# Performance work log

Measured on AMD Instinct MI355X. Metric: run time of the kernel, lower is better.

Reference implementation:

```python
import jax, jax.numpy as jnp
import numpy as np

N0, N1, N2 = 1500, 6000, 4000
F_IN, F_OUT = 32, 32
K00, K0P = 2, 2
K1N, K11, K12, K1P = 2, 2, 2, 2
K2N, K22 = 2, 2


def chebyshev(L, k, x):
    # Chebyshev recursion: T1 = L x, T2 = 2 L T1 - x, T_j = 2 L T_{j-1} - T_{j-2}
    # Returns (n, F, k) stack of T1..Tk (identity term handled by caller).
    t_prev = L @ x
    terms = [t_prev]
    t_pp = x
    for _ in range(k - 1):
        t = 2.0 * (L @ t_prev) - t_pp
        t_pp, t_prev = t_prev, t
        terms.append(t)
    return jnp.stack(terms, axis=2)


def _sym(key, n):
    a = jax.random.normal(key, (n, n), jnp.float32) / jnp.sqrt(jnp.float32(n))
    return 0.5 * (a + a.T)


def setup_inputs():
    key = jax.random.key(0)
    ks = jax.random.split(key, 16)
    x0 = jax.random.normal(ks[0], (N0, F_IN), jnp.float32)
    x1 = jax.random.normal(ks[1], (N1, F_IN), jnp.float32)
    x2 = jax.random.normal(ks[2], (N2, F_IN), jnp.float32)
    B1 = jax.random.normal(ks[3], (N0, N1), jnp.float32) / jnp.sqrt(jnp.float32(N1))
    B2 = jax.random.normal(ks[4], (N1, N2), jnp.float32) / jnp.sqrt(jnp.float32(N2))
    L0 = _sym(ks[5], N0)
    L1l = _sym(ks[6], N1)
    L1u = _sym(ks[7], N1)
    L2 = _sym(ks[8], N2)
    # Degree matrices: diagonal with strictly positive entries (as in real SC data).
    D1 = jnp.diag(jax.random.uniform(ks[9], (N0,), jnp.float32, 0.5, 2.0))
    D2 = jnp.diag(jax.random.uniform(ks[10], (N1,), jnp.float32, 0.5, 2.0))
    D3 = jnp.diag(jax.random.uniform(ks[11], (N2,), jnp.float32, 0.5, 2.0))
    D5 = jnp.diag(jax.random.uniform(ks[12], (N1,), jnp.float32, 0.5, 2.0))
    W0 = jax.random.normal(ks[13], (F_IN, F_OUT, 1 + K00 + 1 + K0P), jnp.float32) * 0.05
    W1 = jax.random.normal(ks[14], (F_IN, F_OUT, 1 + K1N + 1 + K11 + K12 + 1 + K1P), jnp.float32) * 0.05
    W2 = jax.random.normal(ks[15], (F_IN, F_OUT, 1 + K2N + 1 + K22), jnp.float32) * 0.05
    return dict(x0=x0, x1=x1, x2=x2, B1=B1, B2=B2, L0=L0, L1l=L1l, L1u=L1u,
                L2=L2, D1=D1, D2=D2, D3=D3, D5=D5, W0=W0, W1=W1, W2=W2)


def _forward(x0, x1, x2, B1, B2, L0, L1l, L1u, L2, d1_inv, d2, d3, d5_pinv, W0, W1, W2):
    # ---- order 0 ----
    x0p = d1_inv[:, None] * (B1 @ x1)               # inv(D1) @ B1 @ x1
    X0 = jnp.concatenate([x0[:, :, None], chebyshev(L0, K00, x0),
                          x0p[:, :, None], chebyshev(L0, K0P, x0p)], axis=2)
    # ---- order 1 ----
    x1n = d2[:, None] * (B1.T @ (d1_inv[:, None] * x0))  # D2 @ B1.T @ inv(D1) @ x0
    x1p = B2 @ (d3[:, None] * x2)                        # B2 @ D3 @ x2
    X1 = jnp.concatenate([x1n[:, :, None], chebyshev(L1l, K1N, x1n),
                          x1[:, :, None], chebyshev(L1l, K11, x1), chebyshev(L1u, K12, x1),
                          x1p[:, :, None], chebyshev(L1u, K1P, x1p)], axis=2)
    # ---- order 2 ----
    x2n = B2.T @ (d5_pinv[:, None] * x1)                 # B2.T @ pinv(D5) @ x1
    X2 = jnp.concatenate([x2n[:, :, None], chebyshev(L2, K2N, x2n),
                          x2[:, :, None], chebyshev(L2, K22, x2)], axis=2)
    y0 = jax.nn.relu(jnp.einsum('nik,iok->no', X0, W0))
    y1 = jax.nn.relu(jnp.einsum('nik,iok->no', X1, W1))
    y2 = jax.nn.relu(jnp.einsum('nik,iok->no', X2, W2))
    return (y0, y1, y2)


def reference(x0, x1, x2, B1, B2, L0, L1l, L1u, L2, D1, D2, D3, D5, W0, W1, W2):
    # D matrices are diagonal degree matrices; inverse/pinverse of a diagonal
    # matrix is the diagonal of (safe) reciprocals -- identical math to
    # torch.inverse / torch.pinverse on these inputs, without an O(n^3) solve.
    d1_inv = 1.0 / jnp.diag(D1)
    d2 = jnp.diag(D2)
    d3 = jnp.diag(D3)
    d5 = jnp.diag(D5)
    d5_pinv = jnp.where(d5 != 0, 1.0 / d5, 0.0)
    return _forward(x0, x1, x2, B1, B2, L0, L1l, L1u, L2, d1_inv, d2, d3, d5_pinv, W0, W1, W2)
```

## Files before the change

kernel.cpp:

```cpp
#include <hip/hip_runtime.h>
#include <stdint.h>

typedef __attribute__((ext_vector_type(4))) float f32x4;
typedef __attribute__((ext_vector_type(8))) short s16x8;
typedef unsigned short us;

static __device__ __forceinline__ us f2bf(float f) {
  union { float f; uint32_t u; } v; v.f = f;
  uint32_t u = v.u;
  u += 0x7fffu + ((u >> 16) & 1u);
  return (us)(u >> 16);
}

static __device__ __forceinline__ float dval(const float* dv, long r, long dstr, int mode) {
  if (!dv || mode == 0) return 1.f;
  float d = dv[r * dstr];
  if (mode == 2) return (d != 0.f) ? 1.f / d : 0.f;
  return d;
}

static __device__ void tpose_tile(const float* __restrict__ src, long lds_, int n,
                                  const float* __restrict__ dv, long dstr, int mode,
                                  us* __restrict__ dst, int ldn, int tile,
                                  us (*sm)[72]) {
  const int t = threadIdx.x;
  const int r0 = tile * 64;
  {
    const int rr = t & 63;
    const int cg = t >> 6;
    const int gr = r0 + rr;
    float sc = 1.f;
    f32x4 v0 = {0.f, 0.f, 0.f, 0.f}, v1 = {0.f, 0.f, 0.f, 0.f};
    if (gr < n) {
      sc = dval(dv, gr, dstr, mode);
      const float* sp = src + (long)gr * lds_ + cg * 8;
      v0 = *(const f32x4*)sp;
      v1 = *(const f32x4*)(sp + 4);
    }
#pragma unroll
    for (int j = 0; j < 4; ++j) {
      sm[cg * 8 + j][rr] = f2bf(v0[j] * sc);
      sm[cg * 8 + 4 + j][rr] = f2bf(v1[j] * sc);
    }
  }
  __syncthreads();
  {
    const int f = t >> 3;
    const int nc = (t & 7) * 8;
    if (r0 + nc < ldn) {
      s16x8 v = *(const s16x8*)&sm[f][nc];
      *(s16x8*)(dst + (size_t)f * ldn + r0 + nc) = v;
    }
  }
}

static __device__ void convT_tile(const float* __restrict__ in, int ldi, int nI, int nC,
                                  us* __restrict__ outT, int ldoT, int bx, int by,
                                  us (*sT)[72]) {
  const int t = threadIdx.x;
  const int tc0 = bx * 64;
  const int tr0 = by * 64;
  const int c0 = (t & 15) * 4;
  const int r0 = (t >> 4) * 4;
  us ub[4][4];
#pragma unroll
  for (int j = 0; j < 4; ++j) {
    int gr = tr0 + r0 + j;
    f32x4 v = {0.f, 0.f, 0.f, 0.f};
    if (gr < nI) {
      const float* pI = in + (size_t)gr * ldi + tc0 + c0;
      if (tc0 + c0 + 3 < nC) {
        v = *(const f32x4*)pI;
      } else {
#pragma unroll
        for (int jj = 0; jj < 4; ++jj) if (tc0 + c0 + jj < nC) v[jj] = pI[jj];
      }
    }
#pragma unroll
    for (int jj = 0; jj < 4; ++jj) ub[j][jj] = f2bf(v[jj]);
  }
#pragma unroll
  for (int jj = 0; jj < 4; ++jj) {
    union { us u[4]; unsigned long long ll; } w;
#pragma unroll
    for (int j = 0; j < 4; ++j) w.u[j] = ub[j][jj];
    *(unsigned long long*)&sT[c0 + jj][r0] = w.ll;
  }
  __syncthreads();
#pragma unroll
  for (int p = 0; p < 2; ++p) {
    int orow = (t >> 3) + p * 32;
    int rcol = (t & 7) * 8;
    int grow = tc0 + orow;
    int gcol = tr0 + rcol;
    if (grow < nC && gcol < ldoT) {
      union { unsigned long long ll[2]; s16x8 v; } w;
      w.ll[0] = *(const unsigned long long*)&sT[orow][rcol];
      w.ll[1] = *(const unsigned long long*)&sT[orow][rcol + 4];
      *(s16x8*)(outT + (size_t)grow * ldoT + gcol) = w.v;
    }
  }
}

struct TSeg { const float* src; us* dst; int lds_, n, ldn, start; };
struct TPack { TSeg t[8]; int nseg; };

__global__ __launch_bounds__(256) void tpose_batch(TPack P) {
  __shared__ us sm[32][72];
  int b = blockIdx.x;
  int si = P.nseg - 1;
  while (si > 0 && P.t[si].start > b) --si;
  const TSeg s = P.t[si];
  tpose_tile(s.src, s.lds_, s.n, nullptr, 0, 0, s.dst, s.ldn, b - s.start, sm);
}

__global__ __launch_bounds__(256) void prep(
    const float* __restrict__ x0, const float* __restrict__ x1, const float* __restrict__ x2,
    const float* __restrict__ D1, const float* __restrict__ D3, const float* __restrict__ D5,
    const float* __restrict__ W0, const float* __restrict__ W1, const float* __restrict__ W2,
    us* x0T, us* x0dT, us* x1T, us* x1dT, us* x2T, us* x2dT,
    us* W0T, us* W1T, us* W2T,
    float* __restrict__ X0a, float* __restrict__ X1a, float* __restrict__ X2a) {
  __shared__ us sm[32][72];
  int b = blockIdx.x;
  if (b < 24)  { tpose_tile(x0, 32, 1500, nullptr, 0, 0, x0T, 1536, b, sm); return; }
  b -= 24;
  if (b < 24)  { tpose_tile(x0, 32, 1500, D1, 1501, 2, x0dT, 1536, b, sm); return; }
  b -= 24;
  if (b < 94)  { tpose_tile(x1, 32, 6000, nullptr, 0, 0, x1T, 6016, b, sm); return; }
  b -= 94;
  if (b < 94)  { tpose_tile(x1, 32, 6000, D5, 6001, 2, x1dT, 6016, b, sm); return; }
  b -= 94;
  if (b < 64)  { tpose_tile(x2, 32, 4000, nullptr, 0, 0, x2T, 4096, b, sm); return; }
  b -= 64;
  if (b < 64)  { tpose_tile(x2, 32, 4000, D3, 4001, 1, x2dT, 4096, b, sm); return; }
  b -= 64;
  if (b < 3) {
    const float* W = (b == 0) ? W0 : ((b == 1) ? W1 : W2);
    us* dst = (b == 0) ? W0T : ((b == 1) ? W1T : W2T);
    const int K = (b == 1) ? 11 : 6;
    const int C = K * 32;
    const int CP = (b == 1) ? 384 : 192;
    for (int idx = threadIdx.x; idx < 32 * CP; idx += 256) {
      int o = idx / CP, j = idx - o * CP;
      float v = 0.f;
      if (j < C) { int k = j >> 5, i = j & 31; v = W[((long)i * 32 + o) * K + k]; }
      dst[(size_t)o * CP + j] = f2bf(v);
    }
    return;
  }
  b -= 3;
  const long V0 = 1500L * 48, V1 = 6000L * 88, V2 = 4000L * 48;
  for (long i = (long)b * 256 + threadIdx.x; i < V0 + V1 + V2; i += 512L * 256) {
    f32x4 v = {0.f, 0.f, 0.f, 0.f};
    float* dst;
    if (i < V0) {
      long r = i / 48; int c0 = (int)(i - r * 48) * 4;
      if (c0 < 32) v = *(const f32x4*)(x0 + r * 32 + c0);
      dst = X0a + r * 192 + c0;
    } else if (i < V0 + V1) {
      long j = i - V0; long r = j / 88; int c0 = (int)(j - r * 88) * 4;
      if (c0 >= 96 && c0 < 128) v = *(const f32x4*)(x1 + r * 32 + (c0 - 96));
      dst = X1a + r * 352 + c0;
    } else {
      long j = i - V0 - V1; long r = j / 48; int c0 = (int)(j - r * 48) * 4;
      if (c0 >= 96 && c0 < 128) v = *(const f32x4*)(x2 + r * 32 + (c0 - 96));
      dst = X2a + r * 192 + c0;
    }
    *(f32x4*)dst = v;
  }
}

struct Seg {
  const void* A; us* Aout;
  const us* Bt0; const us* Bt1;
  const float* S0; const float* S1; const float* sv;
  float* C0; float* C1;
  float alpha, beta;
  int lda, ldao, ldS, sstr, ldc;
  int n_rows, n_k, ldb, smode, kchunk, tiles, ky, start;
};
struct CSeg { const float* in; us* out; int ldi, nI, nC, ldoT, cx, start; };
struct Mega {
  Seg s[4]; CSeg c[2]; TSeg t[2];
  int nseg, gemm_end, nconv, conv_end, ntp;
};

template <int F, int KSTEP, bool RELU, typename AT>
__global__ __launch_bounds__(256) void mega(Mega P) {
  constexpr int NV = KSTEP / 32;
  __shared__ __align__(16) us lds[64 * (KSTEP == 128 ? 256 : 128)];
  const int b = blockIdx.x;
  if (b >= P.gemm_end) {
    if (b < P.conv_end) {
      int lb = b - P.gemm_end;
      int si = P.nconv - 1;
      while (si > 0 && P.c[si].start > lb) --si;
      const CSeg s = P.c[si];
      int l = lb - s.start;
      convT_tile(s.in, s.ldi, s.nI, s.nC, s.out, s.ldoT, l % s.cx, l / s.cx, (us(*)[72])lds);
    } else {
      int lb = b - P.conv_end;
      int si = P.ntp - 1;
      while (si > 0 && P.t[si].start > lb) --si;
      const TSeg s = P.t[si];
      tpose_tile(s.src, s.lds_, s.n, nullptr, 0, 0, s.dst, s.ldn, lb - s.start, (us(*)[72])lds);
    }
    return;
  }

  us* sA = lds;
  us* sX = lds + 64 * KSTEP;

  int si = P.nseg - 1;
  while (si > 0 && P.s[si].start > b) --si;
  const Seg sg = P.s[si];
  const int local = b - sg.start;
  const int bx = local % sg.tiles;
  const int kidx = local / sg.tiles;

  const AT* __restrict__ A = (const AT*)sg.A;
  const int n_rows = sg.n_rows, n_k = sg.n_k, ldb = sg.ldb;

  const int tid = threadIdx.x;
  const int k_begin = kidx * sg.kchunk;
  const int k_end = min(n_k, k_begin + sg.kchunk);
  const int nsteps = (k_end - k_begin + KSTEP - 1) / KSTEP;

  const int srow = tid >> 2;
  const int sslot = tid & 3;
  const int kc_off = sslot * (KSTEP / 4);
  const long arowg = (long)bx * 64 + srow;
  const bool arow_ok = arowg < n_rows;
  const bool xrow_ok = (F == 64) || (srow < 32);
  const us* xbase = ((srow < 32) ? sg.Bt0 : sg.Bt1) + (size_t)(srow & 31) * ldb;

  f32x4 af[KSTEP / 16];
  s16x8 abf[NV];
  s16x8 xr[NV];

  auto load_tiles = [&](int k0) {
    int kc = k0 + kc_off;
    if constexpr (sizeof(AT) == 4) {
#pragma unroll
      for (int h = 0; h < KSTEP / 16; ++h) af[h] = f32x4{0.f, 0.f, 0.f, 0.f};
      if (arow_ok) {
        const float* ap = (const float*)A + (size_t)arowg * sg.lda + kc;
        if (kc + KSTEP / 4 <= n_k) {
#pragma unroll
          for (int h = 0; h < KSTEP / 16; ++h) af[h] = *(const f32x4*)(ap + 4 * h);
        } else {
#pragma unroll
          for (int h = 0; h < KSTEP / 16; ++h)
#pragma unroll
            for (int j = 0; j < 4; ++j)
              if (kc + 4 * h + j < n_k) af[h][j] = ap[4 * h + j];
        }
      }
    } else {
#pragma unroll
      for (int h = 0; h < NV; ++h) abf[h] = (s16x8)0;
      if (arow_ok) {
        const us* ap = (const us*)A + (size_t)arowg * sg.lda + kc;
        if (kc + KSTEP / 4 <= n_k) {
#pragma unroll
          for (int h = 0; h < NV; ++h) abf[h] = *(const s16x8*)(ap + 8 * h);
        } else {
#pragma unroll
          for (int h = 0; h < NV; ++h)
#pragma unroll
            for (int j = 0; j < 8; ++j)
              if (kc + 8 * h + j < n_k) abf[h][j] = (short)ap[8 * h + j];
        }
      }
    }
    if (xrow_ok) {
#pragma unroll
      for (int h = 0; h < NV; ++h) xr[h] = *(const s16x8*)(xbase + kc + 8 * h);
    }
  };

  load_tiles(k_begin);

  const int wave = tid >> 6;
  const int lane = tid & 63;
  const int g = lane >> 4;
  const int r = lane & 15;

  f32x4 acc[F / 16];
#pragma unroll
  for (int i = 0; i < F / 16; ++i) acc[i] = f32x4{0.f, 0.f, 0.f, 0.f};

  for (int s = 0; s < nsteps; ++s) {
#pragma unroll
    for (int h = 0; h < NV; ++h) {
      s16x8 pk;
      if constexpr (sizeof(AT) == 4) {
#pragma unroll
        for (int j = 0; j < 4; ++j) {
          pk[j] = (short)f2bf(af[2 * h][j]);
          pk[4 + j] = (short)f2bf(af[2 * h + 1][j]);
        }
        if (sg.Aout && arow_ok) {
          *(s16x8*)(sg.Aout + (size_t)arowg * sg.ldao + (k_begin + s * KSTEP + kc_off) + 8 * h) = pk;
        }
      } else {
        pk = abf[h];
      }
      const int ws = ((NV * sslot + h) ^ (srow & 7)) * 8;
      *(s16x8*)&sA[srow * KSTEP + ws] = pk;
      if (xrow_ok) *(s16x8*)&sX[srow * KSTEP + ws] = xr[h];
    }
    __syncthreads();
    if (s + 1 < nsteps) load_tiles(k_begin + (s + 1) * KSTEP);

    const int arow = wave * 16 + r;
#pragma unroll
    for (int kk = 0; kk < NV; ++kk) {
      s16x8 afr = *(s16x8*)&sA[arow * KSTEP + (((kk * 4 + g) ^ (arow & 7)) << 3)];
#pragma unroll
      for (int nt = 0; nt < F / 16; ++nt) {
        int xc = nt * 16 + r;
        s16x8 bfr = *(s16x8*)&sX[xc * KSTEP + (((kk * 4 + g) ^ (xc & 7)) << 3)];
        acc[nt] = __builtin_amdgcn_mfma_f32_16x16x32_bf16(afr, bfr, acc[nt], 0, 0, 0);
      }
    }
    __syncthreads();
  }

  float svv[4];
#pragma unroll
  for (int j = 0; j < 4; ++j) {
    long row = (long)bx * 64 + wave * 16 + g * 4 + j;
    svv[j] = (row < n_rows) ? dval(sg.sv, row, sg.sstr, sg.smode) : 0.f;
  }
#pragma unroll
  for (int nt = 0; nt < F / 16; ++nt) {
    float* C = (F == 64 && nt >= 2) ? sg.C1 : sg.C0;
    const float* S = (F == 64 && nt >= 2) ? sg.S1 : sg.S0;
    int col = ((F == 64) ? (nt & 1) : nt) * 16 + r;
#pragma unroll
    for (int j = 0; j < 4; ++j) {
      long row = (long)bx * 64 + wave * 16 + g * 4 + j;
      if (row < n_rows) {
        float v = sg.alpha * acc[nt][j] * svv[j];
        if (S && (sg.ky == 1 || kidx == 0)) v += sg.beta * S[row * (size_t)sg.ldS + col];
        if (sg.ky > 1) {
          atomicAdd(&C[row * (size_t)sg.ldc + col], v);
        } else {
          if (RELU) v = fmaxf(v, 0.0f);
          C[row * (size_t)sg.ldc + col] = v;
        }
      }
    }
  }
}

__global__ void colcopy(float* __restrict__ dst, const float* __restrict__ src, int n,
                        const float* __restrict__ dv, long dstr, int mode) {
  int idx = blockIdx.x * 256 + threadIdx.x;
  if (idx >= n * 32) return;
  dst[idx] = src[idx] * dval(dv, idx >> 5, dstr, mode);
}
__global__ void scale_ld(float* __restrict__ dst, long ld, int n,
                         const float* __restrict__ dv, long dstr, int mode) {
  int idx = blockIdx.x * 256 + threadIdx.x;
  if (idx >= n * 32) return;
  dst[(size_t)(idx >> 5) * ld + (idx & 31)] *= dval(dv, idx >> 5, dstr, mode);
}
__global__ __launch_bounds__(256) void mm_at(
    const float* __restrict__ A, int lda, int m,
    const float* __restrict__ X,
    float* __restrict__ C, int ldc, int n, int kchunk) {
  const int fg = threadIdx.x & 3;
  const int cg = threadIdx.x >> 2;
  const int c = blockIdx.x * 256 + cg * 4;
  const int k0 = blockIdx.y * kchunk;
  const int k1 = min(m, k0 + kchunk);
  const int f = fg * 8;
  float acc[4][8];
#pragma unroll
  for (int a = 0; a < 4; ++a)
#pragma unroll
    for (int b = 0; b < 8; ++b) acc[a][b] = 0.f;
  for (int k = k0; k < k1; ++k) {
    const float* Ar = A + (size_t)k * lda + c;
    f32x4 a;
    if (c + 3 < n) a = *(const f32x4*)Ar;
    else {
      a = f32x4{0.f, 0.f, 0.f, 0.f};
#pragma unroll
      for (int j = 0; j < 4; ++j) if (c + j < n) a[j] = Ar[j];
    }
    f32x4 xa = *(const f32x4*)(X + (size_t)k * 32 + f);
    f32x4 xb = *(const f32x4*)(X + (size_t)k * 32 + f + 4);
#pragma unroll
    for (int cc = 0; cc < 4; ++cc)
#pragma unroll
      for (int jj = 0; jj < 4; ++jj) {
        acc[cc][jj] += a[cc] * xa[jj];
        acc[cc][4 + jj] += a[cc] * xb[jj];
      }
  }
  if (c >= n) return;
#pragma unroll
  for (int cc = 0; cc < 4; ++cc) {
    if (c + cc >= n) break;
#pragma unroll
    for (int jj = 0; jj < 8; ++jj)
      atomicAdd(&C[(size_t)(c + cc) * ldc + f + jj], acc[cc][jj]);
  }
}


extern "C" void kernel_launch(void* const* d_in, const int* in_sizes, int n_in,
                              void* d_out, int out_size, void* d_ws, size_t ws_size,
                              hipStream_t stream) {
  (void)in_sizes; (void)n_in; (void)out_size;
  const float* x0  = (const float*)d_in[0];
  const float* x1  = (const float*)d_in[1];
  const float* x2  = (const float*)d_in[2];
  const float* B1  = (const float*)d_in[3];
  const float* B2  = (const float*)d_in[4];
  const float* L0  = (const float*)d_in[5];
  const float* L1l = (const float*)d_in[6];
  const float* L1u = (const float*)d_in[7];
  const float* L2  = (const float*)d_in[8];
  const float* D1  = (const float*)d_in[9];
  const float* D2  = (const float*)d_in[10];
  const float* D3  = (const float*)d_in[11];
  const float* D5  = (const float*)d_in[12];
  const float* W0  = (const float*)d_in[13];
  const float* W1  = (const float*)d_in[14];
  const float* W2  = (const float*)d_in[15];
  float* out = (float*)d_out;

  char* p = (char*)d_ws;
  auto alloc = [&](size_t b) { char* r = p; p += (b + 255) & ~(size_t)255; return r; };

  us* x0T   = (us*)alloc((size_t)32 * 1536 * 2);
  us* x0dT  = (us*)alloc((size_t)32 * 1536 * 2);
  us* x1T   = (us*)alloc((size_t)32 * 6016 * 2);
  us* x1dT  = (us*)alloc((size_t)32 * 6016 * 2);
  us* x2T   = (us*)alloc((size_t)32 * 4096 * 2);
  us* x2dT  = (us*)alloc((size_t)32 * 4096 * 2);
  us* x0pT  = (us*)alloc((size_t)32 * 1536 * 2);
  us* x1nT  = (us*)alloc((size_t)32 * 6016 * 2);
  us* x1pT  = (us*)alloc((size_t)32 * 6016 * 2);
  us* x2nT  = (us*)alloc((size_t)32 * 4096 * 2);
  us* T1a0T = (us*)alloc((size_t)32 * 1536 * 2);
  us* T1b0T = (us*)alloc((size_t)32 * 1536 * 2);
  us* T1laT = (us*)alloc((size_t)32 * 6016 * 2);
  us* T1lbT = (us*)alloc((size_t)32 * 6016 * 2);
  us* T1uaT = (us*)alloc((size_t)32 * 6016 * 2);
  us* T1ubT = (us*)alloc((size_t)32 * 6016 * 2);
  us* T1a2T = (us*)alloc((size_t)32 * 4096 * 2);
  us* T1b2T = (us*)alloc((size_t)32 * 4096 * 2);
  us* W0T   = (us*)alloc((size_t)32 * 192 * 2);
  us* W1T   = (us*)alloc((size_t)32 * 384 * 2);
  us* W2T   = (us*)alloc((size_t)32 * 192 * 2);

  float* X0a = (float*)alloc((size_t)1500 * 192 * 4);
  float* X1a = (float*)alloc((size_t)6000 * 352 * 4);
  float* X2a = (float*)alloc((size_t)4000 * 192 * 4);

  float* z0  = (float*)alloc((size_t)1500 * 32 * 4);
  float* sx1 = (float*)alloc((size_t)6000 * 32 * 4);

  size_t used = (size_t)(p - (char*)d_ws);
  const size_t needB  = (size_t)6000 * 1536 * 2 + (size_t)4000 * 6016 * 2 + 1024;
  const size_t needL1 = 2 * (size_t)6000 * 6016 * 2 + 1024;
  const size_t needL02 = (size_t)1500 * 1536 * 2 + (size_t)4000 * 4096 * 2 + 1024;
  bool haveB = used + needB <= ws_size;
  int tier = 0;
  if (haveB) {
    if (used + needB + needL1 + needL02 <= ws_size) tier = 2;
    else if (used + needB + needL1 <= ws_size) tier = 1;
  }
  us *B1t = nullptr, *B2t = nullptr;
  us *L0bf = nullptr, *L1lbf = nullptr, *L1ubf = nullptr, *L2bf = nullptr;
  if (haveB) {
    B1t = (us*)alloc((size_t)6000 * 1536 * 2);
    B2t = (us*)alloc((size_t)4000 * 6016 * 2);
  }
  if (tier >= 1) {
    L1lbf = (us*)alloc((size_t)6000 * 6016 * 2);
    L1ubf = (us*)alloc((size_t)6000 * 6016 * 2);
  }
  if (tier >= 2) {
    L0bf = (us*)alloc((size_t)1500 * 1536 * 2);
    L2bf = (us*)alloc((size_t)4000 * 4096 * 2);
  }

  auto nb = [](long t) { return (unsigned)((t + 255) / 256); };
  auto seg = [](const void* A, us* Aout, int lda, int ldao, int n_rows, int n_k,
                const us* Bt0, const us* Bt1, int ldb,
                float alpha, const float* S0, const float* S1, int ldS, float beta,
                const float* sv, int sstr, int smode,
                float* C0, float* C1, int ldc,
                int kchunk, int tiles, int ky, int start) {
    Seg s;
    s.A = A; s.Aout = Aout; s.Bt0 = Bt0; s.Bt1 = Bt1; s.S0 = S0; s.S1 = S1; s.sv = sv;
    s.C0 = C0; s.C1 = C1; s.alpha = alpha; s.beta = beta;
    s.lda = lda; s.ldao = ldao; s.ldS = ldS; s.sstr = sstr; s.ldc = ldc;
    s.n_rows = n_rows; s.n_k = n_k; s.ldb = ldb; s.smode = smode;
    s.kchunk = kchunk; s.tiles = tiles; s.ky = ky; s.start = start;
    return s;
  };

  prep<<<879, 256, 0, stream>>>(x0, x1, x2, D1, D3, D5, W0, W1, W2,
                                x0T, x0dT, x1T, x1dT, x2T, x2dT, W0T, W1T, W2T,
                                X0a, X1a, X2a);

  {
    Mega P{};
    P.nseg = 2;
    P.s[0] = seg(B1, nullptr, 6000, 0, 1500, 6000, x1T, x1T, 6016,
                 1.f, nullptr, nullptr, 0, 0.f, D1, 1501, 2,
                 X0a + 3 * 32, nullptr, 192, 768, 24, 8, 0);
    P.s[1] = seg(B2, nullptr, 4000, 0, 6000, 4000, x2dT, x2dT, 4096,
                 1.f, nullptr, nullptr, 0, 0.f, nullptr, 0, 0,
                 X1a + 8 * 32, nullptr, 352, 512, 94, 8, 192);
    P.gemm_end = 944;
    if (haveB) {
      P.nconv = 2;
      P.c[0] = CSeg{B1, B1t, 6000, 1500, 6000, 1536, 94, 0};
      P.c[1] = CSeg{B2, B2t, 4000, 6000, 4000, 6016, 63, 2256};
      P.conv_end = 944 + 8178;
    } else {
      P.nconv = 0; P.conv_end = 944;
    }
    P.ntp = 0;
    mega<32, 128, false, float><<<P.conv_end, 256, 0, stream>>>(P);
  }

  if (haveB) {
    Mega P{};
    P.nseg = 2;
    P.s[0] = seg(B1t, nullptr, 1536, 0, 6000, 1536, x0dT, x0dT, 1536,
                 1.f, nullptr, nullptr, 0, 0.f, D2, 6001, 1,
                 X1a + 0 * 32, nullptr, 352, 384, 94, 4, 0);
    P.s[1] = seg(B2t, nullptr, 6016, 0, 4000, 6016, x1dT, x1dT, 6016,
                 1.f, nullptr, nullptr, 0, 0.f, nullptr, 0, 0,
                 X2a + 0 * 32, nullptr, 192, 768, 63, 8, 376);
    P.gemm_end = 880;
    P.nconv = 0; P.conv_end = 880;
    P.ntp = 2;
    P.t[0] = TSeg{X0a + 3 * 32, x0pT, 192, 1500, 1536, 0};
    P.t[1] = TSeg{X1a + 8 * 32, x1pT, 352, 6000, 6016, 24};
    mega<32, 128, false, us><<<998, 256, 0, stream>>>(P);
  } else {
    colcopy<<<nb(1500L * 32), 256, 0, stream>>>(z0, x0, 1500, D1, 1501, 2);
    mm_at<<<dim3(24, 24), 256, 0, stream>>>(B1, 6000, 1500, z0, X1a + 0 * 32, 352, 6000, 63);
    scale_ld<<<nb(6000L * 32), 256, 0, stream>>>(X1a + 0 * 32, 352, 6000, D2, 6001, 1);
    colcopy<<<nb(6000L * 32), 256, 0, stream>>>(sx1, x1, 6000, D5, 6001, 2);
    mm_at<<<dim3(16, 32), 256, 0, stream>>>(B2, 4000, 6000, sx1, X2a + 0 * 32, 192, 4000, 188);
    TPack T{};
    T.nseg = 2;
    T.t[0] = TSeg{X0a + 3 * 32, x0pT, 192, 1500, 1536, 0};
    T.t[1] = TSeg{X1a + 8 * 32, x1pT, 352, 6000, 6016, 24};
    tpose_batch<<<118, 256, 0, stream>>>(T);
  }

  {
    TPack T{};
    T.nseg = 2;
    T.t[0] = TSeg{X1a + 0 * 32, x1nT, 352, 6000, 6016, 0};
    T.t[1] = TSeg{X2a + 0 * 32, x2nT, 192, 4000, 4096, 94};
    tpose_batch<<<158, 256, 0, stream>>>(T);
  }

  {
    Mega P{};
    P.nseg = 4;
    P.s[0] = seg(L0, L0bf, 1500, 1536, 1500, 1500, x0T, x0pT, 1536,
                 1.f, nullptr, nullptr, 0, 0.f, nullptr, 0, 0,
                 X0a + 1 * 32, X0a + 4 * 32, 192, 384, 24, 4, 0);
    P.s[1] = seg(L1l, L1lbf, 6000, 6016, 6000, 6000, x1nT, x1T, 6016,
                 1.f, nullptr, nullptr, 0, 0.f, nullptr, 0, 0,
                 X1a + 1 * 32, X1a + 4 * 32, 352, 768, 94, 8, 96);
    P.s[2] = seg(L1u, L1ubf, 6000, 6016, 6000, 6000, x1T, x1pT, 6016,
                 1.f, nullptr, nullptr, 0, 0.f, nullptr, 0, 0,
                 X1a + 6 * 32, X1a + 9 * 32, 352, 768, 94, 8, 848);
    P.s[3] = seg(L2, L2bf, 4000, 4096, 4000, 4000, x2nT, x2T, 4096,
                 1.f, nullptr, nullptr, 0, 0.f, nullptr, 0, 0,
                 X2a + 1 * 32, X2a + 4 * 32, 192, 512, 63, 8, 1600);
    P.gemm_end = 2104; P.nconv = 0; P.conv_end = 2104; P.ntp = 0;
    mega<64, 128, false, float><<<2104, 256, 0, stream>>>(P);
  }

  {
    TPack T{};
    T.nseg = 8;
    T.t[0] = TSeg{X0a + 1 * 32, T1a0T, 192, 1500, 1536, 0};
    T.t[1] = TSeg{X0a + 4 * 32, T1b0T, 192, 1500, 1536, 24};
    T.t[2] = TSeg{X1a + 1 * 32, T1laT, 352, 6000, 6016, 48};
    T.t[3] = TSeg{X1a + 4 * 32, T1lbT, 352, 6000, 6016, 142};
    T.t[4] = TSeg{X1a + 6 * 32, T1uaT, 352, 6000, 6016, 236};
    T.t[5] = TSeg{X1a + 9 * 32, T1ubT, 352, 6000, 6016, 330};
    T.t[6] = TSeg{X2a + 1 * 32, T1a2T, 192, 4000, 4096, 424};
    T.t[7] = TSeg{X2a + 4 * 32, T1b2T, 192, 4000, 4096, 488};
    tpose_batch<<<552, 256, 0, stream>>>(T);
  }

  {
    if (tier == 2) {
      Mega P{};
      P.nseg = 4;
      P.s[0] = seg(L0bf, nullptr, 1536, 0, 1500, 1536, T1a0T, T1b0T, 1536,
                   2.f, X0a + 0 * 32, X0a + 3 * 32, 192, -1.f, nullptr, 0, 0,
                   X0a + 2 * 32, X0a + 5 * 32, 192, 384, 24, 4, 0);
      P.s[1] = seg(L1lbf, nullptr, 6016, 0, 6000, 6016, T1laT, T1lbT, 6016,
                   2.f, X1a + 0 * 32, X1a + 3 * 32, 352, -1.f, nullptr, 0, 0,
                   X1a + 2 * 32, X1a + 5 * 32, 352, 768, 94, 8, 96);
      P.s[2] = seg(L1ubf, nullptr, 6016, 0, 6000, 6016, T1uaT, T1ubT, 6016,
                   2.f, X1a + 3 * 32, X1a + 8 * 32, 352, -1.f, nullptr, 0, 0,
                   X1a + 7 * 32, X1a + 10 * 32, 352, 768, 94, 8, 848);
      P.s[3] = seg(L2bf, nullptr, 4096, 0, 4000, 4096, T1a2T, T1b2T, 4096,
                   2.f, X2a + 0 * 32, X2a + 3 * 32, 192, -1.f, nullptr, 0, 0,
                   X2a + 2 * 32, X2a + 5 * 32, 192, 512, 63, 8, 1600);
      P.gemm_end = 2104; P.nconv = 0; P.conv_end = 2104; P.ntp = 0;
      mega<64, 128, false, us><<<2104, 256, 0, stream>>>(P);
    } else if (tier == 1) {
      Mega P{};
      P.nseg = 2;
      P.s[0] = seg(L1lbf, nullptr, 6016, 0, 6000, 6016, T1laT, T1lbT, 6016,
                   2.f, X1a + 0 * 32, X1a + 3 * 32, 352, -1.f, nullptr, 0, 0,
                   X1a + 2 * 32, X1a + 5 * 32, 352, 768, 94, 8, 0);
      P.s[1] = seg(L1ubf, nullptr, 6016, 0, 6000, 6016, T1uaT, T1ubT, 6016,
                   2.f, X1a + 3 * 32, X1a + 8 * 32, 352, -1.f, nullptr, 0, 0,
                   X1a + 7 * 32, X1a + 10 * 32, 352, 768, 94, 8, 752);
      P.gemm_end = 1504; P.nconv = 0; P.conv_end = 1504; P.ntp = 0;
      mega<64, 128, false, us><<<1504, 256, 0, stream>>>(P);
      Mega Q{};
      Q.nseg = 2;
      Q.s[0] = seg(L0, nullptr, 1500, 0, 1500, 1500, T1a0T, T1b0T, 1536,
                   2.f, X0a + 0 * 32, X0a + 3 * 32, 192, -1.f, nullptr, 0, 0,
                   X0a + 2 * 32, X0a + 5 * 32, 192, 384, 24, 4, 0);
      Q.s[1] = seg(L2, nullptr, 4000, 0, 4000, 4000, T1a2T, T1b2T, 4096,
                   2.f, X2a + 0 * 32, X2a + 3 * 32, 192, -1.f, nullptr, 0, 0,
                   X2a + 2 * 32, X2a + 5 * 32, 192, 512, 63, 8, 96);
      Q.gemm_end = 600; Q.nconv = 0; Q.conv_end = 600; Q.ntp = 0;
      mega<64, 128, false, float><<<600, 256, 0, stream>>>(Q);
    } else {
      Mega P{};
      P.nseg = 4;
      P.s[0] = seg(L0, nullptr, 1500, 0, 1500, 1500, T1a0T, T1b0T, 1536,
                   2.f, X0a + 0 * 32, X0a + 3 * 32, 192, -1.f, nullptr, 0, 0,
                   X0a + 2 * 32, X0a + 5 * 32, 192, 384, 24, 4, 0);
      P.s[1] = seg(L1l, nullptr, 6000, 0, 6000, 6000, T1laT, T1lbT, 6016,
                   2.f, X1a + 0 * 32, X1a + 3 * 32, 352, -1.f, nullptr, 0, 0,
                   X1a + 2 * 32, X1a + 5 * 32, 352, 768, 94, 8, 96);
      P.s[2] = seg(L1u, nullptr, 6000, 0, 6000, 6000, T1uaT, T1ubT, 6016,
                   2.f, X1a + 3 * 32, X1a + 8 * 32, 352, -1.f, nullptr, 0, 0,
                   X1a + 7 * 32, X1a + 10 * 32, 352, 768, 94, 8, 848);
      P.s[3] = seg(L2, nullptr, 4000, 0, 4000, 4000, T1a2T, T1b2T, 4096,
                   2.f, X2a + 0 * 32, X2a + 3 * 32, 192, -1.f, nullptr, 0, 0,
                   X2a + 2 * 32, X2a + 5 * 32, 192, 512, 63, 8, 1600);
      P.gemm_end = 2104; P.nconv = 0; P.conv_end = 2104; P.ntp = 0;
      mega<64, 128, false, float><<<2104, 256, 0, stream>>>(P);
    }
  }

  {
    Mega P{};
    P.nseg = 3;
    P.s[0] = seg(X0a, nullptr, 192, 0, 1500, 192, W0T, W0T, 192,
                 1.f, nullptr, nullptr, 0, 0.f, nullptr, 0, 0,
                 out, nullptr, 32, 192, 24, 1, 0);
    P.s[1] = seg(X1a, nullptr, 352, 0, 6000, 352, W1T, W1T, 384,
                 1.f, nullptr, nullptr, 0, 0.f, nullptr, 0, 0,
                 out + 48000, nullptr, 32, 384, 94, 1, 24);
    P.s[2] = seg(X2a, nullptr, 192, 0, 4000, 192, W2T, W2T, 192,
                 1.f, nullptr, nullptr, 0, 0.f, nullptr, 0, 0,
                 out + 240000, nullptr, 32, 192, 63, 1, 118);
    P.gemm_end = 181; P.nconv = 0; P.conv_end = 181; P.ntp = 0;
    mega<32, 64, true, float><<<181, 256, 0, stream>>>(P);
  }
}
```

Measured before the change: 350.4 us.

## Store bf16 operands pre-swizzled in MFMA fragment order and drop LDS staging

All bf16 intermediate buffers (transposed features, converted B/L matrices, weights) are now written in a tiled layout that matches the 16x16x32 MFMA lane fragment order. The GEMM kernel can then load fragments straight from global memory into registers, with no shared-memory staging or barriers. It uses a two-stage register double buffer with 64-wide K steps. The goal is to remove LDS round trips and syncthreads from the dense Laplacian/incidence GEMMs. The cost is that each wave issues scattered 16-byte global loads without cross-wave reuse of the X operand through LDS, and all producer kernels must follow the new layout exactly.

```diff
diff --git a/kernel.cpp b/kernel.cpp
--- a/kernel.cpp
+++ b/kernel.cpp
@@ -18,6 +18,7 @@
   if (mode == 2) return (d != 0.f) ? 1.f / d : 0.f;
   return d;
 }
+
 
 static __device__ void tpose_tile(const float* __restrict__ src, long lds_, int n,
                                   const float* __restrict__ dv, long dstr, int mode,
@@ -46,16 +47,18 @@
   __syncthreads();
   {
     const int f = t >> 3;
-    const int nc = (t & 7) * 8;
-    if (r0 + nc < ldn) {
-      s16x8 v = *(const s16x8*)&sm[f][nc];
-      *(s16x8*)(dst + (size_t)f * ldn + r0 + nc) = v;
-    }
-  }
+    const int low = t & 7;
+    const int kk = low >> 2, q = low & 3;
+    const int lane = (f & 15) | (q << 4);
+    const int nt = f >> 4;
+    size_t off = (size_t)tile * 2048 + (size_t)(kk * 2 + nt) * 512 + (size_t)lane * 8;
+    *(s16x8*)(dst + off) = *(const s16x8*)&sm[f][low * 8];
+  }
+  (void)ldn;
 }
 
 static __device__ void convT_tile(const float* __restrict__ in, int ldi, int nI, int nC,
-                                  us* __restrict__ outT, int ldoT, int bx, int by,
+                                  us* __restrict__ outT, int nkstep, int bx, int by,
                                   us (*sT)[72]) {
   const int t = threadIdx.x;
   const int tc0 = bx * 64;
@@ -89,16 +92,13 @@
   __syncthreads();
 #pragma unroll
   for (int p = 0; p < 2; ++p) {
-    int orow = (t >> 3) + p * 32;
-    int rcol = (t & 7) * 8;
-    int grow = tc0 + orow;
-    int gcol = tr0 + rcol;
-    if (grow < nC && gcol < ldoT) {
-      union { unsigned long long ll[2]; s16x8 v; } w;
-      w.ll[0] = *(const unsigned long long*)&sT[orow][rcol];
-      w.ll[1] = *(const unsigned long long*)&sT[orow][rcol + 4];
-      *(s16x8*)(outT + (size_t)grow * ldoT + gcol) = w.v;
-    }
+    const int orow = (t >> 3) + p * 32;
+    const int low = t & 7;
+    const int kk = low >> 2, q = low & 3;
+    const int lane = (orow & 15) | (q << 4);
+    size_t off = ((size_t)((tc0 >> 4) + (orow >> 4)) * nkstep + (tr0 >> 6)) * 1024
+               + (size_t)kk * 512 + (size_t)lane * 8;
+    *(s16x8*)(outT + off) = *(const s16x8*)&sT[orow][low * 8];
   }
 }
 
@@ -142,10 +142,12 @@
     const int C = K * 32;
     const int CP = (b == 1) ? 384 : 192;
     for (int idx = threadIdx.x; idx < 32 * CP; idx += 256) {
-      int o = idx / CP, j = idx - o * CP;
+      int o = idx / CP, k = idx - o * CP;
       float v = 0.f;
-      if (j < C) { int k = j >> 5, i = j & 31; v = W[((long)i * 32 + o) * K + k]; }
-      dst[(size_t)o * CP + j] = f2bf(v);
+      if (k < C) { int kw = k >> 5, i = k & 31; v = W[((long)i * 32 + o) * K + kw]; }
+      size_t off = (size_t)(k >> 6) * 2048 + (size_t)(((k >> 5) & 1) * 2 + (o >> 4)) * 512
+                 + (size_t)((o & 15) | (((k >> 3) & 3) << 4)) * 8 + (k & 7);
+      dst[off] = f2bf(v);
     }
     return;
   }
@@ -178,18 +180,17 @@
   float* C0; float* C1;
   float alpha, beta;
   int lda, ldao, ldS, sstr, ldc;
-  int n_rows, n_k, ldb, smode, kchunk, tiles, ky, start;
+  int n_rows, n_k, smode, kchunk, tiles, ky, start;
 };
-struct CSeg { const float* in; us* out; int ldi, nI, nC, ldoT, cx, start; };
+struct CSeg { const float* in; us* out; int ldi, nI, nC, nkstep, cx, start; };
 struct Mega {
   Seg s[4]; CSeg c[2]; TSeg t[2];
   int nseg, gemm_end, nconv, conv_end, ntp;
 };
 
-template <int F, int KSTEP, bool RELU, typename AT>
+template <int F, bool RELU, int AMODE>
 __global__ __launch_bounds__(256) void mega(Mega P) {
-  constexpr int NV = KSTEP / 32;
-  __shared__ __align__(16) us lds[64 * (KSTEP == 128 ? 256 : 128)];
+  __shared__ us sm[64][72];
   const int b = blockIdx.x;
   if (b >= P.gemm_end) {
     if (b < P.conv_end) {
@@ -198,20 +199,19 @@
       while (si > 0 && P.c[si].start > lb) --si;
       const CSeg s = P.c[si];
       int l = lb - s.start;
-      convT_tile(s.in, s.ldi, s.nI, s.nC, s.out, s.ldoT, l % s.cx, l / s.cx, (us(*)[72])lds);
+      convT_tile(s.in, s.ldi, s.nI, s.nC, s.out, s.nkstep, l % s.cx, l / s.cx, sm);
     } else {
       int lb = b - P.conv_end;
       int si = P.ntp - 1;
       while (si > 0 && P.t[si].start > lb) --si;
       const TSeg s = P.t[si];
-      tpose_tile(s.src, s.lds_, s.n, nullptr, 0, 0, s.dst, s.ldn, lb - s.start, (us(*)[72])lds);
+      tpose_tile(s.src, s.lds_, s.n, nullptr, 0, 0, s.dst, s.ldn, lb - s.start,
+                 (us(*)[72])sm);
     }
     return;
   }
 
-  us* sA = lds;
-  us* sX = lds + 64 * KSTEP;
-
+  constexpr int NT = F / 16;
   int si = P.nseg - 1;
   while (si > 0 && P.s[si].start > b) --si;
   const Seg sg = P.s[si];
@@ -219,129 +219,118 @@
   const int bx = local % sg.tiles;
   const int kidx = local / sg.tiles;
 
-  const AT* __restrict__ A = (const AT*)sg.A;
-  const int n_rows = sg.n_rows, n_k = sg.n_k, ldb = sg.ldb;
-
   const int tid = threadIdx.x;
+  const int w = tid >> 6;
+  const int lane = tid & 63;
+  const int r = lane & 15;
+  const int g = lane >> 4;
+
+  const int n_rows = sg.n_rows, n_k = sg.n_k;
+  const long arow = (long)bx * 64 + w * 16 + r;
+  const bool arow_ok = arow < n_rows;
+  const int rowblk = bx * 4 + w;
+
   const int k_begin = kidx * sg.kchunk;
   const int k_end = min(n_k, k_begin + sg.kchunk);
-  const int nsteps = (k_end - k_begin + KSTEP - 1) / KSTEP;
-
-  const int srow = tid >> 2;
-  const int sslot = tid & 3;
-  const int kc_off = sslot * (KSTEP / 4);
-  const long arowg = (long)bx * 64 + srow;
-  const bool arow_ok = arowg < n_rows;
-  const bool xrow_ok = (F == 64) || (srow < 32);
-  const us* xbase = ((srow < 32) ? sg.Bt0 : sg.Bt1) + (size_t)(srow & 31) * ldb;
-
-  f32x4 af[KSTEP / 16];
-  s16x8 abf[NV];
-  s16x8 xr[NV];
-
-  auto load_tiles = [&](int k0) {
-    int kc = k0 + kc_off;
-    if constexpr (sizeof(AT) == 4) {
-#pragma unroll
-      for (int h = 0; h < KSTEP / 16; ++h) af[h] = f32x4{0.f, 0.f, 0.f, 0.f};
-      if (arow_ok) {
-        const float* ap = (const float*)A + (size_t)arowg * sg.lda + kc;
-        if (kc + KSTEP / 4 <= n_k) {
-#pragma unroll
-          for (int h = 0; h < KSTEP / 16; ++h) af[h] = *(const f32x4*)(ap + 4 * h);
-        } else {
-#pragma unroll
-          for (int h = 0; h < KSTEP / 16; ++h)
-#pragma unroll
-            for (int j = 0; j < 4; ++j)
-              if (kc + 4 * h + j < n_k) af[h][j] = ap[4 * h + j];
+  const int nsteps = (k_end - k_begin + 63) >> 6;
+
+  const float* Af = nullptr;
+  const us* Ad = nullptr;
+  if (AMODE == 0) Af = (const float*)sg.A + (size_t)(arow_ok ? arow : 0) * sg.lda;
+  else Ad = (const us*)sg.A + ((size_t)rowblk * sg.lda) * 1024 + lane * 8;
+
+  f32x4 aA[4], aB[4];
+  s16x8 abA[2], abB[2];
+  s16x8 xA[2 * NT], xB[2 * NT];
+
+  auto LD = [&](int s, f32x4* av, s16x8* abv, s16x8* xv) {
+    const int k0 = k_begin + s * 64;
+    const int kstep = k0 >> 6;
+    if constexpr (AMODE == 0) {
+#pragma unroll
+      for (int kk = 0; kk < 2; ++kk) {
+        const int kc = k0 + kk * 32 + g * 8;
+        f32x4 u0 = {0.f, 0.f, 0.f, 0.f}, u1 = {0.f, 0.f, 0.f, 0.f};
+        if (arow_ok) {
+          const float* ap = Af + kc;
+          if (kc + 8 <= n_k) {
+            u0 = *(const f32x4*)ap; u1 = *(const f32x4*)(ap + 4);
+          } else {
+#pragma unroll
+            for (int j = 0; j < 4; ++j) {
+              if (kc + j < n_k) u0[j] = ap[j];
+              if (kc + 4 + j < n_k) u1[j] = ap[4 + j];
+            }
+          }
         }
+        av[kk * 2] = u0; av[kk * 2 + 1] = u1;
       }
     } else {
-#pragma unroll
-      for (int h = 0; h < NV; ++h) abf[h] = (s16x8)0;
-      if (arow_ok) {
-        const us* ap = (const us*)A + (size_t)arowg * sg.lda + kc;
-        if (kc + KSTEP / 4 <= n_k) {
-#pragma unroll
-          for (int h = 0; h < NV; ++h) abf[h] = *(const s16x8*)(ap + 8 * h);
-        } else {
-#pragma unroll
-          for (int h = 0; h < NV; ++h)
-#pragma unroll
-            for (int j = 0; j < 8; ++j)
-              if (kc + 8 * h + j < n_k) abf[h][j] = (short)ap[8 * h + j];
-        }
+      const us* ap = Ad + (size_t)kstep * 1024;
+      abv[0] = *(const s16x8*)ap;
+      abv[1] = *(const s16x8*)(ap + 512);
+    }
+#pragma unroll
+    for (int kk = 0; kk < 2; ++kk)
+#pragma unroll
+      for (int nt = 0; nt < NT; ++nt) {
+        const us* xp = (NT == 4 && nt >= 2) ? sg.Bt1 : sg.Bt0;
+        xv[kk * NT + nt] = *(const s16x8*)(xp + ((size_t)kstep * 4 + kk * 2 + (nt & 1)) * 512
+                                           + lane * 8);
       }
-    }
-    if (xrow_ok) {
-#pragma unroll
-      for (int h = 0; h < NV; ++h) xr[h] = *(const s16x8*)(xbase + kc + 8 * h);
-    }
   };
 
-  load_tiles(k_begin);
-
-  const int wave = tid >> 6;
-  const int lane = tid & 63;
-  const int g = lane >> 4;
-  const int r = lane & 15;
-
-  f32x4 acc[F / 16];
-#pragma unroll
-  for (int i = 0; i < F / 16; ++i) acc[i] = f32x4{0.f, 0.f, 0.f, 0.f};
-
-  for (int s = 0; s < nsteps; ++s) {
-#pragma unroll
-    for (int h = 0; h < NV; ++h) {
-      s16x8 pk;
-      if constexpr (sizeof(AT) == 4) {
-#pragma unroll
-        for (int j = 0; j < 4; ++j) {
-          pk[j] = (short)f2bf(af[2 * h][j]);
-          pk[4 + j] = (short)f2bf(af[2 * h + 1][j]);
-        }
-        if (sg.Aout && arow_ok) {
-          *(s16x8*)(sg.Aout + (size_t)arowg * sg.ldao + (k_begin + s * KSTEP + kc_off) + 8 * h) = pk;
-        }
-      } else {
-        pk = abf[h];
+  f32x4 acc[NT];
+#pragma unroll
+  for (int i = 0; i < NT; ++i) acc[i] = f32x4{0.f, 0.f, 0.f, 0.f};
+
+  auto CMP = [&](int s, f32x4* av, s16x8* abv, s16x8* xv) {
+    s16x8 pa0, pa1;
+    if constexpr (AMODE == 0) {
+#pragma unroll
+      for (int j = 0; j < 4; ++j) {
+        pa0[j] = (short)f2bf(av[0][j]); pa0[4 + j] = (short)f2bf(av[1][j]);
+        pa1[j] = (short)f2bf(av[2][j]); pa1[4 + j] = (short)f2bf(av[3][j]);
       }
-      const int ws = ((NV * sslot + h) ^ (srow & 7)) * 8;
-      *(s16x8*)&sA[srow * KSTEP + ws] = pk;
-      if (xrow_ok) *(s16x8*)&sX[srow * KSTEP + ws] = xr[h];
-    }
-    __syncthreads();
-    if (s + 1 < nsteps) load_tiles(k_begin + (s + 1) * KSTEP);
-
-    const int arow = wave * 16 + r;
-#pragma unroll
-    for (int kk = 0; kk < NV; ++kk) {
-      s16x8 afr = *(s16x8*)&sA[arow * KSTEP + (((kk * 4 + g) ^ (arow & 7)) << 3)];
-#pragma unroll
-      for (int nt = 0; nt < F / 16; ++nt) {
-        int xc = nt * 16 + r;
-        s16x8 bfr = *(s16x8*)&sX[xc * KSTEP + (((kk * 4 + g) ^ (xc & 7)) << 3)];
-        acc[nt] = __builtin_amdgcn_mfma_f32_16x16x32_bf16(afr, bfr, acc[nt], 0, 0, 0);
+      if (sg.Aout && arow_ok) {
+        const int kstep = (k_begin + s * 64) >> 6;
+        us* q = sg.Aout + ((size_t)rowblk * sg.ldao + kstep) * 1024 + lane * 8;
+        *(s16x8*)q = pa0;
+        *(s16x8*)(q + 512) = pa1;
       }
-    }
-    __syncthreads();
-  }
+    } else { pa0 = abv[0]; pa1 = abv[1]; (void)s; }
+#pragma unroll
+    for (int nt = 0; nt < NT; ++nt)
+      acc[nt] = __builtin_amdgcn_mfma_f32_16x16x32_bf16(pa0, xv[nt], acc[nt], 0, 0, 0);
+#pragma unroll
+    for (int nt = 0; nt < NT; ++nt)
+      acc[nt] = __builtin_amdgcn_mfma_f32_16x16x32_bf16(pa1, xv[NT + nt], acc[nt], 0, 0, 0);
+  };
+
+  if (nsteps > 0) LD(0, aA, abA, xA);
+  int s = 0;
+  for (; s + 1 < nsteps; s += 2) {
+    LD(s + 1, aB, abB, xB);
+    CMP(s, aA, abA, xA);
+    if (s + 2 < nsteps) LD(s + 2, aA, abA, xA);
+    CMP(s + 1, aB, abB, xB);
+  }
+  if (s < nsteps) CMP(s, aA, abA, xA);
 
   float svv[4];
 #pragma unroll
   for (int j = 0; j < 4; ++j) {
-    long row = (long)bx * 64 + wave * 16 + g * 4 + j;
+    long row = (long)bx * 64 + w * 16 + g * 4 + j;
     svv[j] = (row < n_rows) ? dval(sg.sv, row, sg.sstr, sg.smode) : 0.f;
   }
 #pragma unroll
-  for (int nt = 0; nt < F / 16; ++nt) {
+  for (int nt = 0; nt < NT; ++nt) {
     float* C = (F == 64 && nt >= 2) ? sg.C1 : sg.C0;
     const float* S = (F == 64 && nt >= 2) ? sg.S1 : sg.S0;
     int col = ((F == 64) ? (nt & 1) : nt) * 16 + r;
 #pragma unroll
     for (int j = 0; j < 4; ++j) {
-      long row = (long)bx * 64 + wave * 16 + g * 4 + j;
+      long row = (long)bx * 64 + w * 16 + g * 4 + j;
       if (row < n_rows) {
         float v = sg.alpha * acc[nt][j] * svv[j];
         if (S && (sg.ky == 1 || kidx == 0)) v += sg.beta * S[row * (size_t)sg.ldS + col];
@@ -382,7 +371,7 @@
 #pragma unroll
   for (int a = 0; a < 4; ++a)
 #pragma unroll
-    for (int b = 0; b < 8; ++b) acc[a][b] = 0.f;
+    for (int bb = 0; bb < 8; ++bb) acc[a][bb] = 0.f;
   for (int k = k0; k < k1; ++k) {
     const float* Ar = A + (size_t)k * lda + c;
     f32x4 a;
@@ -436,29 +425,29 @@
   float* out = (float*)d_out;
 
   char* p = (char*)d_ws;
-  auto alloc = [&](size_t b) { char* r = p; p += (b + 255) & ~(size_t)255; return r; };
-
-  us* x0T   = (us*)alloc((size_t)32 * 1536 * 2);
-  us* x0dT  = (us*)alloc((size_t)32 * 1536 * 2);
-  us* x1T   = (us*)alloc((size_t)32 * 6016 * 2);
-  us* x1dT  = (us*)alloc((size_t)32 * 6016 * 2);
-  us* x2T   = (us*)alloc((size_t)32 * 4096 * 2);
-  us* x2dT  = (us*)alloc((size_t)32 * 4096 * 2);
-  us* x0pT  = (us*)alloc((size_t)32 * 1536 * 2);
-  us* x1nT  = (us*)alloc((size_t)32 * 6016 * 2);
-  us* x1pT  = (us*)alloc((size_t)32 * 6016 * 2);
-  us* x2nT  = (us*)alloc((size_t)32 * 4096 * 2);
-  us* T1a0T = (us*)alloc((size_t)32 * 1536 * 2);
-  us* T1b0T = (us*)alloc((size_t)32 * 1536 * 2);
-  us* T1laT = (us*)alloc((size_t)32 * 6016 * 2);
-  us* T1lbT = (us*)alloc((size_t)32 * 6016 * 2);
-  us* T1uaT = (us*)alloc((size_t)32 * 6016 * 2);
-  us* T1ubT = (us*)alloc((size_t)32 * 6016 * 2);
-  us* T1a2T = (us*)alloc((size_t)32 * 4096 * 2);
-  us* T1b2T = (us*)alloc((size_t)32 * 4096 * 2);
-  us* W0T   = (us*)alloc((size_t)32 * 192 * 2);
-  us* W1T   = (us*)alloc((size_t)32 * 384 * 2);
-  us* W2T   = (us*)alloc((size_t)32 * 192 * 2);
+  auto alloc = [&](size_t bsz) { char* r = p; p += (bsz + 255) & ~(size_t)255; return r; };
+
+  us* x0T   = (us*)alloc((size_t)24 * 4096);
+  us* x0dT  = (us*)alloc((size_t)24 * 4096);
+  us* x1T   = (us*)alloc((size_t)94 * 4096);
+  us* x1dT  = (us*)alloc((size_t)94 * 4096);
+  us* x2T   = (us*)alloc((size_t)64 * 4096);
+  us* x2dT  = (us*)alloc((size_t)64 * 4096);
+  us* x0pT  = (us*)alloc((size_t)24 * 4096);
+  us* x1nT  = (us*)alloc((size_t)94 * 4096);
+  us* x1pT  = (us*)alloc((size_t)94 * 4096);
+  us* x2nT  = (us*)alloc((size_t)64 * 4096);
+  us* T1a0T = (us*)alloc((size_t)24 * 4096);
+  us* T1b0T = (us*)alloc((size_t)24 * 4096);
+  us* T1laT = (us*)alloc((size_t)94 * 4096);
+  us* T1lbT = (us*)alloc((size_t)94 * 4096);
+  us* T1uaT = (us*)alloc((size_t)94 * 4096);
+  us* T1ubT = (us*)alloc((size_t)94 * 4096);
+  us* T1a2T = (us*)alloc((size_t)64 * 4096);
+  us* T1b2T = (us*)alloc((size_t)64 * 4096);
+  us* W0T   = (us*)alloc((size_t)3 * 4096);
+  us* W1T   = (us*)alloc((size_t)6 * 4096);
+  us* W2T   = (us*)alloc((size_t)3 * 4096);
 
   float* X0a = (float*)alloc((size_t)1500 * 192 * 4);
   float* X1a = (float*)alloc((size_t)6000 * 352 * 4);
@@ -467,10 +456,16 @@
   float* z0  = (float*)alloc((size_t)1500 * 32 * 4);
   float* sx1 = (float*)alloc((size_t)6000 * 32 * 4);
 
+  const size_t szB1t = (size_t)376 * 24 * 2048;
+  const size_t szB2t = (size_t)252 * 94 * 2048;
+  const size_t szL0  = (size_t)96 * 24 * 2048;
+  const size_t szL1  = (size_t)376 * 94 * 2048;
+  const size_t szL2  = (size_t)252 * 64 * 2048;
+
   size_t used = (size_t)(p - (char*)d_ws);
-  const size_t needB  = (size_t)6000 * 1536 * 2 + (size_t)4000 * 6016 * 2 + 1024;
-  const size_t needL1 = 2 * (size_t)6000 * 6016 * 2 + 1024;
-  const size_t needL02 = (size_t)1500 * 1536 * 2 + (size_t)4000 * 4096 * 2 + 1024;
+  const size_t needB  = szB1t + szB2t + 1024;
+  const size_t needL1 = 2 * szL1 + 1024;
+  const size_t needL02 = szL0 + szL2 + 1024;
   bool haveB = used + needB <= ws_size;
   int tier = 0;
   if (haveB) {
@@ -479,22 +474,13 @@
   }
   us *B1t = nullptr, *B2t = nullptr;
   us *L0bf = nullptr, *L1lbf = nullptr, *L1ubf = nullptr, *L2bf = nullptr;
-  if (haveB) {
-    B1t = (us*)alloc((size_t)6000 * 1536 * 2);
-    B2t = (us*)alloc((size_t)4000 * 6016 * 2);
-  }
-  if (tier >= 1) {
-    L1lbf = (us*)alloc((size_t)6000 * 6016 * 2);
-    L1ubf = (us*)alloc((size_t)6000 * 6016 * 2);
-  }
-  if (tier >= 2) {
-    L0bf = (us*)alloc((size_t)1500 * 1536 * 2);
-    L2bf = (us*)alloc((size_t)4000 * 4096 * 2);
-  }
+  if (haveB) { B1t = (us*)alloc(szB1t); B2t = (us*)alloc(szB2t); }
+  if (tier >= 1) { L1lbf = (us*)alloc(szL1); L1ubf = (us*)alloc(szL1); }
+  if (tier >= 2) { L0bf = (us*)alloc(szL0); L2bf = (us*)alloc(szL2); }
 
   auto nb = [](long t) { return (unsigned)((t + 255) / 256); };
   auto seg = [](const void* A, us* Aout, int lda, int ldao, int n_rows, int n_k,
-                const us* Bt0, const us* Bt1, int ldb,
+                const us* Bt0, const us* Bt1,
                 float alpha, const float* S0, const float* S1, int ldS, float beta,
                 const float* sv, int sstr, int smode,
                 float* C0, float* C1, int ldc,
@@ -503,7 +489,7 @@
     s.A = A; s.Aout = Aout; s.Bt0 = Bt0; s.Bt1 = Bt1; s.S0 = S0; s.S1 = S1; s.sv = sv;
     s.C0 = C0; s.C1 = C1; s.alpha = alpha; s.beta = beta;
     s.lda = lda; s.ldao = ldao; s.ldS = ldS; s.sstr = sstr; s.ldc = ldc;
-    s.n_rows = n_rows; s.n_k = n_k; s.ldb = ldb; s.smode = smode;
+    s.n_rows = n_rows; s.n_k = n_k; s.smode = smode;
     s.kchunk = kchunk; s.tiles = tiles; s.ky = ky; s.start = start;
     return s;
   };
@@ -515,32 +501,32 @@
   {
     Mega P{};
     P.nseg = 2;
-    P.s[0] = seg(B1, nullptr, 6000, 0, 1500, 6000, x1T, x1T, 6016,
+    P.s[0] = seg(B1, nullptr, 6000, 0, 1500, 6000, x1T, x1T,
                  1.f, nullptr, nullptr, 0, 0.f, D1, 1501, 2,
                  X0a + 3 * 32, nullptr, 192, 768, 24, 8, 0);
-    P.s[1] = seg(B2, nullptr, 4000, 0, 6000, 4000, x2dT, x2dT, 4096,
+    P.s[1] = seg(B2, nullptr, 4000, 0, 6000, 4000, x2dT, x2dT,
                  1.f, nullptr, nullptr, 0, 0.f, nullptr, 0, 0,
                  X1a + 8 * 32, nullptr, 352, 512, 94, 8, 192);
     P.gemm_end = 944;
     if (haveB) {
       P.nconv = 2;
-      P.c[0] = CSeg{B1, B1t, 6000, 1500, 6000, 1536, 94, 0};
-      P.c[1] = CSeg{B2, B2t, 4000, 6000, 4000, 6016, 63, 2256};
-      P.conv_end = 944 + 8178;
+      P.c[0] = CSeg{B1, B1t, 6000, 1500, 6000, 24, 94, 0};
+      P.c[1] = CSeg{B2, B2t, 4000, 6000, 4000, 94, 63, 2256};
+      P.conv_end = 944 + 2256 + 5922;
     } else {
       P.nconv = 0; P.conv_end = 944;
     }
     P.ntp = 0;
-    mega<32, 128, false, float><<<P.conv_end, 256, 0, stream>>>(P);
+    mega<32, false, 0><<<P.conv_end, 256, 0, stream>>>(P);
   }
 
   if (haveB) {
     Mega P{};
     P.nseg = 2;
-    P.s[0] = seg(B1t, nullptr, 1536, 0, 6000, 1536, x0dT, x0dT, 1536,
+    P.s[0] = seg(B1t, nullptr, 24, 0, 6000, 1536, x0dT, x0dT,
                  1.f, nullptr, nullptr, 0, 0.f, D2, 6001, 1,
                  X1a + 0 * 32, nullptr, 352, 384, 94, 4, 0);
-    P.s[1] = seg(B2t, nullptr, 6016, 0, 4000, 6016, x1dT, x1dT, 6016,
+    P.s[1] = seg(B2t, nullptr, 94, 0, 4000, 6016, x1dT, x1dT,
                  1.f, nullptr, nullptr, 0, 0.f, nullptr, 0, 0,
                  X2a + 0 * 32, nullptr, 192, 768, 63, 8, 376);
     P.gemm_end = 880;
@@ -548,7 +534,7 @@
     P.ntp = 2;
     P.t[0] = TSeg{X0a + 3 * 32, x0pT, 192, 1500, 1536, 0};
     P.t[1] = TSeg{X1a + 8 * 32, x1pT, 352, 6000, 6016, 24};
-    mega<32, 128, false, us><<<998, 256, 0, stream>>>(P);
+    mega<32, false, 1><<<998, 256, 0, stream>>>(P);
   } else {
     colcopy<<<nb(1500L * 32), 256, 0, stream>>>(z0, x0, 1500, D1, 1501, 2);
     mm_at<<<dim3(24, 24), 256, 0, stream>>>(B1, 6000, 1500, z0, X1a + 0 * 32, 352, 6000, 63);
@@ -573,20 +559,20 @@
   {
     Mega P{};
     P.nseg = 4;
-    P.s[0] = seg(L0, L0bf, 1500, 1536, 1500, 1500, x0T, x0pT, 1536,
+    P.s[0] = seg(L0, L0bf, 1500, 24, 1500, 1500, x0T, x0pT,
                  1.f, nullptr, nullptr, 0, 0.f, nullptr, 0, 0,
                  X0a + 1 * 32, X0a + 4 * 32, 192, 384, 24, 4, 0);
-    P.s[1] = seg(L1l, L1lbf, 6000, 6016, 6000, 6000, x1nT, x1T, 6016,
+    P.s[1] = seg(L1l, L1lbf, 6000, 94, 6000, 6000, x1nT, x1T,
                  1.f, nullptr, nullptr, 0, 0.f, nullptr, 0, 0,
                  X1a + 1 * 32, X1a + 4 * 32, 352, 768, 94, 8, 96);
-    P.s[2] = seg(L1u, L1ubf, 6000, 6016, 6000, 6000, x1T, x1pT, 6016,
+    P.s[2] = seg(L1u, L1ubf, 6000, 94, 6000, 6000, x1T, x1pT,
                  1.f, nullptr, nullptr, 0, 0.f, nullptr, 0, 0,
                  X1a + 6 * 32, X1a + 9 * 32, 352, 768, 94, 8, 848);
-    P.s[3] = seg(L2, L2bf, 4000, 4096, 4000, 4000, x2nT, x2T, 4096,
+    P.s[3] = seg(L2, L2bf, 4000, 64, 4000, 4000, x2nT, x2T,
                  1.f, nullptr, nullptr, 0, 0.f, nullptr, 0, 0,
                  X2a + 1 * 32, X2a + 4 * 32, 192, 512, 63, 8, 1600);
     P.gemm_end = 2104; P.nconv = 0; P.conv_end = 2104; P.ntp = 0;
-    mega<64, 128, false, float><<<2104, 256, 0, stream>>>(P);
+    mega<64, false, 0><<<2104, 256, 0, stream>>>(P);
   }
 
   {
@@ -607,74 +593,74 @@
     if (tier == 2) {
       Mega P{};
       P.nseg = 4;
-      P.s[0] = seg(L0bf, nullptr, 1536, 0, 1500, 1536, T1a0T, T1b0T, 1536,
+      P.s[0] = seg(L0bf, nullptr, 24, 0, 1500, 1536, T1a0T, T1b0T,
                    2.f, X0a + 0 * 32, X0a + 3 * 32, 192, -1.f, nullptr, 0, 0,
                    X0a + 2 * 32, X0a + 5 * 32, 192, 384, 24, 4, 0);
-      P.s[1] = seg(L1lbf, nullptr, 6016, 0, 6000, 6016, T1laT, T1lbT, 6016,
+      P.s[1] = seg(L1lbf, nullptr, 94, 0, 6000, 6016, T1laT, T1lbT,
                    2.f, X1a + 0 * 32, X1a + 3 * 32, 352, -1.f, nullptr, 0, 0,
                    X1a + 2 * 32, X1a + 5 * 32, 352, 768, 94, 8, 96);
-      P.s[2] = seg(L1ubf, nullptr, 6016, 0, 6000, 6016, T1uaT, T1ubT, 6016,
+      P.s[2] = seg(L1ubf, nullptr, 94, 0, 6000, 6016, T1uaT, T1ubT,
                    2.f, X1a + 3 * 32, X1a + 8 * 32, 352, -1.f, nullptr, 0, 0,
                    X1a + 7 * 32, X1a + 10 * 32, 352, 768, 94, 8, 848);
-      P.s[3] = seg(L2bf, nullptr, 4096, 0, 4000, 4096, T1a2T, T1b2T, 4096,
+      P.s[3] = seg(L2bf, nullptr, 64, 0, 4000, 4096, T1a2T, T1b2T,
                    2.f, X2a + 0 * 32, X2a + 3 * 32, 192, -1.f, nullptr, 0, 0,
                    X2a + 2 * 32, X2a + 5 * 32, 192, 512, 63, 8, 1600);
       P.gemm_end = 2104; P.nconv = 0; P.conv_end = 2104; P.ntp = 0;
-      mega<64, 128, false, us><<<2104, 256, 0, stream>>>(P);
+      mega<64, false, 1><<<2104, 256, 0, stream>>>(P);
     } else if (tier == 1) {
       Mega P{};
       P.nseg = 2;
-      P.s[0] = seg(L1lbf, nullptr, 6016, 0, 6000, 6016, T1laT, T1lbT, 6016,
+      P.s[0] = seg(L1lbf, nullptr, 94, 0, 6000, 6016, T1laT, T1lbT,
                    2.f, X1a + 0 * 32, X1a + 3 * 32, 352, -1.f, nullptr, 0, 0,
                    X1a + 2 * 32, X1a + 5 * 32, 352, 768, 94, 8, 0);
-      P.s[1] = seg(L1ubf, nullptr, 6016, 0, 6000, 6016, T1uaT, T1ubT, 6016,
+      P.s[1] = seg(L1ubf, nullptr, 94, 0, 6000, 6016, T1uaT, T1ubT,
                    2.f, X1a + 3 * 32, X1a + 8 * 32, 352, -1.f, nullptr, 0, 0,
                    X1a + 7 * 32, X1a + 10 * 32, 352, 768, 94, 8, 752);
       P.gemm_end = 1504; P.nconv = 0; P.conv_end = 1504; P.ntp = 0;
-      mega<64, 128, false, us><<<1504, 256, 0, stream>>>(P);
+      mega<64, false, 1><<<1504, 256, 0, stream>>>(P);
       Mega Q{};
       Q.nseg = 2;
-      Q.s[0] = seg(L0, nullptr, 1500, 0, 1500, 1500, T1a0T, T1b0T, 1536,
+      Q.s[0] = seg(L0, nullptr, 1500, 0, 1500, 1500, T1a0T, T1b0T,
                    2.f, X0a + 0 * 32, X0a + 3 * 32, 192, -1.f, nullptr, 0, 0,
                    X0a + 2 * 32, X0a + 5 * 32, 192, 384, 24, 4, 0);
-      Q.s[1] = seg(L2, nullptr, 4000, 0, 4000, 4000, T1a2T, T1b2T, 4096,
+      Q.s[1] = seg(L2, nullptr, 4000, 0, 4000, 4000, T1a2T, T1b2T,
                    2.f, X2a + 0 * 32, X2a + 3 * 32, 192, -1.f, nullptr, 0, 0,
                    X2a + 2 * 32, X2a + 5 * 32, 192, 512, 63, 8, 96);
       Q.gemm_end = 600; Q.nconv = 0; Q.conv_end = 600; Q.ntp = 0;
-      mega<64, 128, false, float><<<600, 256, 0, stream>>>(Q);
+      mega<64, false, 0><<<600, 256, 0, stream>>>(Q);
     } else {
       Mega P{};
       P.nseg = 4;
-      P.s[0] = seg(L0, nullptr, 1500, 0, 1500, 1500, T1a0T, T1b0T, 1536,
+      P.s[0] = seg(L0, nullptr, 1500, 0, 1500, 1500, T1a0T, T1b0T,
                    2.f, X0a + 0 * 32, X0a + 3 * 32, 192, -1.f, nullptr, 0, 0,
                    X0a + 2 * 32, X0a + 5 * 32, 192, 384, 24, 4, 0);
-      P.s[1] = seg(L1l, nullptr, 6000, 0, 6000, 6000, T1laT, T1lbT, 6016,
+      P.s[1] = seg(L1l, nullptr, 6000, 0, 6000, 6000, T1laT, T1lbT,
                    2.f, X1a + 0 * 32, X1a + 3 * 32, 352, -1.f, nullptr, 0, 0,
                    X1a + 2 * 32, X1a + 5 * 32, 352, 768, 94, 8, 96);
-      P.s[2] = seg(L1u, nullptr, 6000, 0, 6000, 6000, T1uaT, T1ubT, 6016,
+      P.s[2] = seg(L1u, nullptr, 6000, 0, 6000, 6000, T1uaT, T1ubT,
                    2.f, X1a + 3 * 32, X1a + 8 * 32, 352, -1.f, nullptr, 0, 0,
                    X1a + 7 * 32, X1a + 10 * 32, 352, 768, 94, 8, 848);
-      P.s[3] = seg(L2, nullptr, 4000, 0, 4000, 4000, T1a2T, T1b2T, 4096,
+      P.s[3] = seg(L2, nullptr, 4000, 0, 4000, 4000, T1a2T, T1b2T,
                    2.f, X2a + 0 * 32, X2a + 3 * 32, 192, -1.f, nullptr, 0, 0,
                    X2a + 2 * 32, X2a + 5 * 32, 192, 512, 63, 8, 1600);
       P.gemm_end = 2104; P.nconv = 0; P.conv_end = 2104; P.ntp = 0;
-      mega<64, 128, false, float><<<2104, 256, 0, stream>>>(P);
+      mega<64, false, 0><<<2104, 256, 0, stream>>>(P);
     }
   }
 
   {
     Mega P{};
     P.nseg = 3;
-    P.s[0] = seg(X0a, nullptr, 192, 0, 1500, 192, W0T, W0T, 192,
+    P.s[0] = seg(X0a, nullptr, 192, 0, 1500, 192, W0T, W0T,
                  1.f, nullptr, nullptr, 0, 0.f, nullptr, 0, 0,
                  out, nullptr, 32, 192, 24, 1, 0);
-    P.s[1] = seg(X1a, nullptr, 352, 0, 6000, 352, W1T, W1T, 384,
+    P.s[1] = seg(X1a, nullptr, 352, 0, 6000, 352, W1T, W1T,
                  1.f, nullptr, nullptr, 0, 0.f, nullptr, 0, 0,
                  out + 48000, nullptr, 32, 384, 94, 1, 24);
-    P.s[2] = seg(X2a, nullptr, 192, 0, 4000, 192, W2T, W2T, 192,
+    P.s[2] = seg(X2a, nullptr, 192, 0, 4000, 192, W2T, W2T,
                  1.f, nullptr, nullptr, 0, 0.f, nullptr, 0, 0,
                  out + 240000, nullptr, 32, 192, 63, 1, 118);
     P.gemm_end = 181; P.nconv = 0; P.conv_end = 181; P.ntp = 0;
-    mega<32, 64, true, float><<<181, 256, 0, stream>>>(P);
-  }
-}
+    mega<32, true, 0><<<181, 256, 0, stream>>>(P);
+  }
+}
```

Result: faster. 337.7 us (-3.6%).
